# Optimization experiments

Measured on AMD Instinct MI355X. Metric: run time of the kernel, lower is better.

Reference implementation:

```python
import jax, jax.numpy as jnp
import numpy as np

N_QUBITS = 4
Q_DEPTH = 6
Q_DELTA = 0.01


def _conv1d(x, w, b):
    # x: (B, Cin, L), w: (Cout, Cin, 3), padding=1
    y = jax.lax.conv_general_dilated(x, w, window_strides=(1,), padding=[(1, 1)],
                                     dimension_numbers=('NCH', 'OIH', 'NCH'))
    return y + b[None, :, None]


def _maxpool2(x):
    B, C, L = x.shape
    return x.reshape(B, C, L // 2, 2).max(axis=-1)


def _take(state, i, axis):
    return jax.lax.index_in_dim(state, i, axis, keepdims=False)


def _apply_ry(state, theta, wire):
    # state: (B, 2, 2, 2, 2); theta: scalar (shared weight) or (B,) (per-sample)
    half = theta * 0.5
    c, s = jnp.cos(half), jnp.sin(half)
    if c.ndim == 1:  # per-sample angles -> broadcast over remaining qubit axes
        c = c.reshape(-1, 1, 1, 1)
        s = s.reshape(-1, 1, 1, 1)
    ax = wire + 1
    s0 = _take(state, 0, ax)
    s1 = _take(state, 1, ax)
    return jnp.stack([c * s0 - s * s1, s * s0 + c * s1], axis=ax)


def _apply_cnot(state, ctrl, tgt):
    cax, tax = ctrl + 1, tgt + 1
    a0 = jax.lax.slice_in_dim(state, 0, 1, axis=cax)
    a1 = jax.lax.slice_in_dim(state, 1, 2, axis=cax)
    return jnp.concatenate([a0, jnp.flip(a1, axis=tax)], axis=cax)


def _quantum_forward(q_in, q_params):
    # Batched 4-qubit state-vector simulation (PennyLane default.qubit semantics,
    # wire 0 = most significant -> axis wire+1 of (B,2,2,2,2) state).
    B = q_in.shape[0]
    # H layer on |0000> -> uniform amplitude 1/4
    state = jnp.full((B, 2, 2, 2, 2), 0.25, dtype=q_in.dtype)
    for w in range(N_QUBITS):
        state = _apply_ry(state, q_in[:, w], w)
    qw = q_params.reshape(Q_DEPTH, N_QUBITS)
    for k in range(Q_DEPTH):
        # entangling layer: CNOT(0,1), CNOT(2,3), then CNOT(1,2)
        state = _apply_cnot(state, 0, 1)
        state = _apply_cnot(state, 2, 3)
        state = _apply_cnot(state, 1, 2)
        for w in range(N_QUBITS):
            state = _apply_ry(state, qw[k, w], w)
    probs = state * state  # real amplitudes throughout (H as initial |+>^n, RY, CNOT)
    zs = [(_take(probs, 0, q + 1) - _take(probs, 1, q + 1)).sum(axis=(1, 2, 3))
          for q in range(N_QUBITS)]
    return jnp.stack(zs, axis=1)  # (B, 4) <Z_q>


def setup_inputs() -> dict:
    key = jax.random.key(0)
    ks = jax.random.split(key, 12)
    B, F = 32768, 64
    FLAT = 64 * (F // 4)  # 1024
    return {
        'x': jax.random.normal(ks[0], (B, F), jnp.float32),
        'conv1_w': jax.random.normal(ks[1], (32, 1, 3), jnp.float32) * 0.3,
        'conv1_b': jax.random.normal(ks[2], (32,), jnp.float32) * 0.05,
        'conv2_w': jax.random.normal(ks[3], (64, 32, 3), jnp.float32) * 0.05,
        'conv2_b': jax.random.normal(ks[4], (64,), jnp.float32) * 0.05,
        'fc_w': jax.random.normal(ks[5], (FLAT, 64), jnp.float32) * (1.0 / np.sqrt(FLAT)),
        'fc_b': jax.random.normal(ks[6], (64,), jnp.float32) * 0.05,
        'pre_w': jax.random.normal(ks[7], (64, N_QUBITS), jnp.float32) * 0.125,
        'pre_b': jax.random.normal(ks[8], (N_QUBITS,), jnp.float32) * 0.05,
        'q_params': Q_DELTA * jax.random.normal(ks[9], (Q_DEPTH * N_QUBITS,), jnp.float32),
        'post_w': jax.random.normal(ks[10], (N_QUBITS, 1), jnp.float32) * 0.5,
        'post_b': jax.random.normal(ks[11], (1,), jnp.float32) * 0.05,
    }


def reference(x, conv1_w, conv1_b, conv2_w, conv2_b, fc_w, fc_b,
              pre_w, pre_b, q_params, post_w, post_b):
    h = x[:, None, :]  # (B, 1, F)
    h = _maxpool2(jax.nn.relu(_conv1d(h, conv1_w, conv1_b)))   # (B, 32, F/2)
    h = _maxpool2(jax.nn.relu(_conv1d(h, conv2_w, conv2_b)))   # (B, 64, F/4)
    h = h.reshape(h.shape[0], -1)                              # (B, 1024)
    h = jax.nn.relu(h @ fc_w + fc_b)                           # (B, 64)
    q_in = jnp.tanh(h @ pre_w + pre_b) * (np.pi / 2.0)         # (B, 4)
    q_out = _quantum_forward(q_in, q_params)                   # (B, 4)
    return jax.nn.sigmoid(q_out @ post_w + post_b)             # (B, 1)
```

## Files before the change

### kernel.cpp

```cpp
#include <hip/hip_runtime.h>
#include <math.h>

typedef unsigned short u16;
typedef unsigned int u32;
typedef __attribute__((ext_vector_type(8))) short bf16x8;
typedef __attribute__((ext_vector_type(4))) float f32x4;

__device__ __forceinline__ u16 f32_to_bf16(float f) {
    u32 u = __float_as_uint(f);
    u32 r = u + 0x7FFFu + ((u >> 16) & 1u);
    return (u16)(r >> 16);
}
__device__ __forceinline__ u32 pack2(u16 a, u16 b) { return (u32)a | ((u32)b << 16); }

__device__ __forceinline__ u32 rne_bits(float f) {
    u32 u = __float_as_uint(f);
    return u + 0x7FFFu + ((u >> 16) & 1u);
}
__device__ __forceinline__ u32 pack_rne(float a, float b) {
    return __builtin_amdgcn_perm(rne_bits(b), rne_bits(a), 0x07060302u);
}

__device__ __forceinline__ float fast_tanh(float x) {
    float e = __expf(2.f * x);
    return 1.f - 2.f / (e + 1.f);
}

template<int STRIDE>
__device__ __forceinline__ void ry_gate(float st[16], float theta) {
    float s, c;
    sincosf(theta * 0.5f, &s, &c);
#pragma unroll
    for (int i = 0; i < 16; ++i) {
        if (i & STRIDE) continue;
        float s0 = st[i], s1 = st[i | STRIDE];
        st[i]          = c * s0 - s * s1;
        st[i | STRIDE] = fmaf(s, s0, c * s1);
    }
}
template<int CS, int TS>
__device__ __forceinline__ void cnot_gate(float st[16]) {
#pragma unroll
    for (int i = 0; i < 16; ++i) {
        if ((i & CS) && !(i & TS)) {
            float tmp = st[i]; st[i] = st[i | TS]; st[i | TS] = tmp;
        }
    }
}

__global__ __launch_bounds__(256) void prep_kernel(
    const float* __restrict__ fcw, const float* __restrict__ w2,
    const float* __restrict__ qp,
    u16* __restrict__ whi, u16* __restrict__ w2b, float* __restrict__ Mg)
{
    const int f  = blockIdx.x;
    const int k0 = threadIdx.x * 4;
    u16 hv[4];
#pragma unroll
    for (int i = 0; i < 4; ++i) {
        int k  = k0 + i;
        int op = k >> 6, oc = k & 63;
        hv[i] = f32_to_bf16(fcw[(size_t)(oc * 16 + op) * 64 + f]);
    }
    *(uint2*)(whi + (size_t)f * 1024 + k0) = make_uint2(pack2(hv[0], hv[1]), pack2(hv[2], hv[3]));

    if (threadIdx.x < 96) {
        const int j  = threadIdx.x;
        const int ic = j / 3, t = j - ic * 3;
        w2b[(t * 64 + f) * 32 + ic] = f32_to_bf16(w2[f * 96 + j]);
    }

    if (blockIdx.x == 0 && threadIdx.x < 16) {
        const int j = threadIdx.x;
        float st[16];
#pragma unroll
        for (int i = 0; i < 16; ++i) st[i] = (i == j) ? 1.f : 0.f;
        for (int k = 0; k < 6; ++k) {
            cnot_gate<8, 4>(st);
            cnot_gate<2, 1>(st);
            cnot_gate<4, 2>(st);
            ry_gate<8>(st, qp[k * 4 + 0]);
            ry_gate<4>(st, qp[k * 4 + 1]);
            ry_gate<2>(st, qp[k * 4 + 2]);
            ry_gate<1>(st, qp[k * 4 + 3]);
        }
#pragma unroll
        for (int i = 0; i < 16; ++i) Mg[i * 16 + j] = st[i];
    }
}

__global__ __launch_bounds__(1024, 4) void fused_kernel(
    const float* __restrict__ x,
    const float* __restrict__ w1, const float* __restrict__ b1,
    const u16* __restrict__ w2b, const float* __restrict__ b2,
    const u16* __restrict__ whi,
    const float* __restrict__ fcb,
    const float* __restrict__ prew, const float* __restrict__ preb,
    const float* __restrict__ postw, const float* __restrict__ postb,
    const float* __restrict__ Mg,
    float* __restrict__ out)
{
    __shared__ __align__(16) u16 c1h[32 * 1384];
    __shared__ float prews[256];
    __shared__ float Ms[16][17];

    const int tid  = threadIdx.x;
    const int bs   = blockIdx.x * 32;
    const int wv   = tid >> 6, lane = tid & 63;
    const int lr   = lane & 15, lq = lane >> 4;

    if (tid < 256) {
        prews[tid] = prew[tid];
        Ms[tid >> 4][tid & 15] = Mg[tid];
    }

    {
        const int s1 = tid >> 5;
        const int pp = tid & 31;
        const float* xb = x + (size_t)(bs + s1) * 64;
        const int j = 2 * pp;
        float xm1 = (j == 0)  ? 0.f : xb[j - 1];
        float x0  = xb[j];
        float x1  = xb[j + 1];
        float xp2 = (j == 62) ? 0.f : xb[j + 2];

        u16* sbase = c1h + s1 * 1384;
        if (pp == 0 || pp == 31) {
            uint4 z = make_uint4(0, 0, 0, 0);
            uint4* zr = (uint4*)(sbase + (pp == 0 ? 0 : 33) * 40);
            zr[0] = z; zr[1] = z; zr[2] = z; zr[3] = z;
        }
        u32 row[16];
#pragma unroll
        for (int icp = 0; icp < 16; ++icp) {
            float v[2];
#pragma unroll
            for (int h2 = 0; h2 < 2; ++h2) {
                int ic = icp * 2 + h2;
                float wa = w1[ic * 3], wb = w1[ic * 3 + 1], wc = w1[ic * 3 + 2], bb = b1[ic];
                float y0 = bb + wa * xm1 + wb * x0 + wc * x1;
                float y1 = bb + wa * x0  + wb * x1 + wc * xp2;
                v[h2] = fmaxf(fmaxf(y0, y1), 0.f);
            }
            row[icp] = pack_rne(v[0], v[1]);
        }
        uint4* d = (uint4*)(sbase + (1 + pp) * 40);
        d[0] = make_uint4(row[0],  row[1],  row[2],  row[3]);
        d[1] = make_uint4(row[4],  row[5],  row[6],  row[7]);
        d[2] = make_uint4(row[8],  row[9],  row[10], row[11]);
        d[3] = make_uint4(row[12], row[13], row[14], row[15]);
    }

    bf16x8 af[3][4];
#pragma unroll
    for (int t = 0; t < 3; ++t)
#pragma unroll
        for (int mt = 0; mt < 4; ++mt)
            af[t][mt] = *(const bf16x8*)(w2b + (size_t)(t * 64 + mt * 16 + lr) * 32 + lq * 8);
    f32x4 bias2[4];
#pragma unroll
    for (int mt = 0; mt < 4; ++mt)
        bias2[mt] = *(const f32x4*)(b2 + mt * 16 + lq * 4);
    __syncthreads();

#pragma unroll
    for (int nt = 0; nt < 4; ++nt) {
        const int s  = wv * 2 + (nt >> 1);
        const int qb = (nt & 1) * 16;
        const u16* bp = c1h + s * 1384 + (qb + lr) * 40 + lq * 8;
        bf16x8 bf0 = *(const bf16x8*)(bp);
        bf16x8 bf1 = *(const bf16x8*)(bp + 40);
        bf16x8 bf2 = *(const bf16x8*)(bp + 80);
        const int op = (qb + lr) >> 1;
#pragma unroll
        for (int mt = 0; mt < 4; ++mt) {
            f32x4 acc = __builtin_amdgcn_mfma_f32_16x16x32_bf16(af[0][mt], bf0, bias2[mt], 0, 0, 0);
            acc = __builtin_amdgcn_mfma_f32_16x16x32_bf16(af[1][mt], bf1, acc, 0, 0, 0);
            acc = __builtin_amdgcn_mfma_f32_16x16x32_bf16(af[2][mt], bf2, acc, 0, 0, 0);
            float p0 = fmaxf(fmaxf(acc[0], __shfl_xor(acc[0], 1)), 0.f);
            float p1 = fmaxf(fmaxf(acc[1], __shfl_xor(acc[1], 1)), 0.f);
            float p2 = fmaxf(fmaxf(acc[2], __shfl_xor(acc[2], 1)), 0.f);
            float p3 = fmaxf(fmaxf(acc[3], __shfl_xor(acc[3], 1)), 0.f);
            if (!(lane & 1)) {
                *(uint2*)(c1h + s * 1384 + op * 72 + mt * 16 + lq * 4) =
                    make_uint2(pack_rne(p0, p1), pack_rne(p2, p3));
            }
        }
    }
    __syncthreads();

    if (wv < 4) {
        const int n0 = wv * 16;
        const float fbias = fcb[n0 + lr];
        f32x4 facc0 = {0.f, 0.f, 0.f, 0.f};
        f32x4 facc1 = {0.f, 0.f, 0.f, 0.f};
        const u16* ab0 = c1h + (size_t)lr * 1384 + lq * 8;
        const u16* ab1 = c1h + (size_t)(16 + lr) * 1384 + lq * 8;
        const u16* bh  = whi + (size_t)(n0 + lr) * 1024 + lq * 8;
#pragma unroll 8
        for (int kc = 0; kc < 32; ++kc) {
            const int aoff = (kc >> 1) * 72 + (kc & 1) * 32;
            bf16x8 a0 = *(const bf16x8*)(ab0 + aoff);
            bf16x8 a1 = *(const bf16x8*)(ab1 + aoff);
            bf16x8 fh = *(const bf16x8*)(bh + kc * 32);
            facc0 = __builtin_amdgcn_mfma_f32_16x16x32_bf16(a0, fh, facc0, 0, 0, 0);
            facc1 = __builtin_amdgcn_mfma_f32_16x16x32_bf16(a1, fh, facc1, 0, 0, 0);
        }
#pragma unroll
        for (int r = 0; r < 4; ++r) {
            ((float*)(c1h + (size_t)(lq * 4 + r) * 1384 + 1152))[n0 + lr] =
                fmaxf(facc0[r] + fbias, 0.f);
            ((float*)(c1h + (size_t)(16 + lq * 4 + r) * 1384 + 1152))[n0 + lr] =
                fmaxf(facc1[r] + fbias, 0.f);
        }
    }
    __syncthreads();

    if (lane < 8) {
        const int L = lane & 3;
        const int s = wv * 2 + (lane >> 2);
        const float* hfl = (const float*)(c1h + (size_t)s * 1384 + 1152);

        float a0 = 0.f, a1 = 0.f, a2 = 0.f, a3 = 0.f;
#pragma unroll
        for (int i2 = 0; i2 < 4; ++i2) {
            float4 hv = *(const float4*)(hfl + L * 16 + i2 * 4);
#pragma unroll
            for (int c = 0; c < 4; ++c) {
                int ff = L * 16 + i2 * 4 + c;
                float4 pw = *(const float4*)&prews[ff * 4];
                float hx = (c == 0) ? hv.x : (c == 1) ? hv.y : (c == 2) ? hv.z : hv.w;
                a0 = fmaf(hx, pw.x, a0);
                a1 = fmaf(hx, pw.y, a1);
                a2 = fmaf(hx, pw.z, a2);
                a3 = fmaf(hx, pw.w, a3);
            }
        }
        a0 += __shfl_xor(a0, 1); a0 += __shfl_xor(a0, 2);
        a1 += __shfl_xor(a1, 1); a1 += __shfl_xor(a1, 2);
        a2 += __shfl_xor(a2, 1); a2 += __shfl_xor(a2, 2);
        a3 += __shfl_xor(a3, 1); a3 += __shfl_xor(a3, 2);

        const float HP = 1.5707963267948966f;
        float qin[4] = { fast_tanh(a0 + preb[0]) * HP, fast_tanh(a1 + preb[1]) * HP,
                         fast_tanh(a2 + preb[2]) * HP, fast_tanh(a3 + preb[3]) * HP };

        float va[4], vb[4];
        const float RS = 0.70710678118654752f;
#pragma unroll
        for (int w = 0; w < 4; ++w) {
            float sw, cw;
            __sincosf(qin[w] * 0.5f, &sw, &cw);
            va[w] = (cw - sw) * RS;
            vb[w] = (sw + cw) * RS;
        }
        float sv[16];
#pragma unroll
        for (int jj = 0; jj < 16; ++jj) {
            float t = (jj & 8) ? vb[0] : va[0];
            t *= (jj & 4) ? vb[1] : va[1];
            t *= (jj & 2) ? vb[2] : va[2];
            t *= (jj & 1) ? vb[3] : va[3];
            sv[jj] = t;
        }
        float z0 = 0.f, z1 = 0.f, z2 = 0.f, z3 = 0.f;
#pragma unroll
        for (int rr = 0; rr < 4; ++rr) {
            const int r = L * 4 + rr;
            float m = 0.f;
#pragma unroll
            for (int jj = 0; jj < 16; ++jj) m = fmaf(Ms[r][jj], sv[jj], m);
            float p = m * m;
            z0 += (r & 8) ? -p : p;
            z1 += (r & 4) ? -p : p;
            z2 += (r & 2) ? -p : p;
            z3 += (r & 1) ? -p : p;
        }
        z0 += __shfl_xor(z0, 1); z0 += __shfl_xor(z0, 2);
        z1 += __shfl_xor(z1, 1); z1 += __shfl_xor(z1, 2);
        z2 += __shfl_xor(z2, 1); z2 += __shfl_xor(z2, 2);
        z3 += __shfl_xor(z3, 1); z3 += __shfl_xor(z3, 2);

        if (L == 0) {
            float t = postb[0] + z0 * postw[0] + z1 * postw[1] + z2 * postw[2] + z3 * postw[3];
            out[bs + s] = 1.f / (1.f + __expf(-t));
        }
    }
}

extern "C" void kernel_launch(void* const* d_in, const int* in_sizes, int n_in,
                              void* d_out, int out_size, void* d_ws, size_t ws_size,
                              hipStream_t stream) {
    const float* x     = (const float*)d_in[0];
    const float* w1    = (const float*)d_in[1];
    const float* b1    = (const float*)d_in[2];
    const float* w2    = (const float*)d_in[3];
    const float* b2    = (const float*)d_in[4];
    const float* fcw   = (const float*)d_in[5];
    const float* fcb   = (const float*)d_in[6];
    const float* prew  = (const float*)d_in[7];
    const float* preb  = (const float*)d_in[8];
    const float* qp    = (const float*)d_in[9];
    const float* postw = (const float*)d_in[10];
    const float* postb = (const float*)d_in[11];
    float* out = (float*)d_out;

    u16*   fwhi = (u16*)d_ws;
    float* Mg   = (float*)((char*)d_ws + 131072);
    u16*   w2b  = (u16*)((char*)d_ws + 132096);

    const int B = in_sizes[0] / 64;

    prep_kernel<<<dim3(64), dim3(256), 0, stream>>>(fcw, w2, qp, fwhi, w2b, Mg);
    fused_kernel<<<dim3(B / 32), dim3(1024), 0, stream>>>(x, w1, b1, w2b, b2,
                                                          fwhi, fcb, prew, preb,
                                                          postw, postb, Mg, out);
}
```

Before: 146.4 us.

## Shrink fused kernel blocks to 8 samples and swap MFMA operand roles

The fused kernel now runs 256-thread blocks that each handle 8 samples instead of 1024-thread blocks handling 32. The shared staging buffer shrinks to match, which allows more resident blocks and more blocks in flight. The conv2 MFMA swaps its A and B operands so the maxpool pair lands inside one lane's accumulator, removing the cross-lane shuffles, though outputs are now written as scalar 16-bit stores. In the FC stage every wave runs a single MFMA with the weight as the A operand, but half of each tile's 16 columns duplicate the 8 samples, wasting MFMA work and reloading FC weights once per 8 samples instead of per 32.

```diff
diff --git a/kernel.cpp b/kernel.cpp
--- a/kernel.cpp
+++ b/kernel.cpp
@@ -16,9 +16,6 @@
 __device__ __forceinline__ u32 rne_bits(float f) {
     u32 u = __float_as_uint(f);
     return u + 0x7FFFu + ((u >> 16) & 1u);
-}
-__device__ __forceinline__ u32 pack_rne(float a, float b) {
-    return __builtin_amdgcn_perm(rne_bits(b), rne_bits(a), 0x07060302u);
 }
 
 __device__ __forceinline__ float fast_tanh(float x) {
@@ -89,7 +86,7 @@
     }
 }
 
-__global__ __launch_bounds__(1024, 4) void fused_kernel(
+__global__ __launch_bounds__(256, 5) void fused_kernel(
     const float* __restrict__ x,
     const float* __restrict__ w1, const float* __restrict__ b1,
     const u16* __restrict__ w2b, const float* __restrict__ b2,
@@ -100,19 +97,17 @@
     const float* __restrict__ Mg,
     float* __restrict__ out)
 {
-    __shared__ __align__(16) u16 c1h[32 * 1384];
+    __shared__ __align__(16) u16 c1h[8 * 1384];
     __shared__ float prews[256];
     __shared__ float Ms[16][17];
 
     const int tid  = threadIdx.x;
-    const int bs   = blockIdx.x * 32;
+    const int bs   = blockIdx.x * 8;
     const int wv   = tid >> 6, lane = tid & 63;
     const int lr   = lane & 15, lq = lane >> 4;
 
-    if (tid < 256) {
-        prews[tid] = prew[tid];
-        Ms[tid >> 4][tid & 15] = Mg[tid];
-    }
+    prews[tid] = prew[tid];
+    Ms[tid >> 4][tid & 15] = Mg[tid];
 
     {
         const int s1 = tid >> 5;
@@ -142,7 +137,7 @@
                 float y1 = bb + wa * x0  + wb * x1 + wc * xp2;
                 v[h2] = fmaxf(fmaxf(y0, y1), 0.f);
             }
-            row[icp] = pack_rne(v[0], v[1]);
+            row[icp] = __builtin_amdgcn_perm(rne_bits(v[1]), rne_bits(v[0]), 0x07060302u);
         }
         uint4* d = (uint4*)(sbase + (1 + pp) * 40);
         d[0] = make_uint4(row[0],  row[1],  row[2],  row[3]);
@@ -157,10 +152,10 @@
 #pragma unroll
         for (int mt = 0; mt < 4; ++mt)
             af[t][mt] = *(const bf16x8*)(w2b + (size_t)(t * 64 + mt * 16 + lr) * 32 + lq * 8);
-    f32x4 bias2[4];
+    float biasv[4];
 #pragma unroll
     for (int mt = 0; mt < 4; ++mt)
-        bias2[mt] = *(const f32x4*)(b2 + mt * 16 + lq * 4);
+        biasv[mt] = b2[mt * 16 + lr];
     __syncthreads();
 
 #pragma unroll
@@ -171,47 +166,40 @@
         bf16x8 bf0 = *(const bf16x8*)(bp);
         bf16x8 bf1 = *(const bf16x8*)(bp + 40);
         bf16x8 bf2 = *(const bf16x8*)(bp + 80);
-        const int op = (qb + lr) >> 1;
+        const int op0 = (qb >> 1) + lq * 2;
 #pragma unroll
         for (int mt = 0; mt < 4; ++mt) {
-            f32x4 acc = __builtin_amdgcn_mfma_f32_16x16x32_bf16(af[0][mt], bf0, bias2[mt], 0, 0, 0);
-            acc = __builtin_amdgcn_mfma_f32_16x16x32_bf16(af[1][mt], bf1, acc, 0, 0, 0);
-            acc = __builtin_amdgcn_mfma_f32_16x16x32_bf16(af[2][mt], bf2, acc, 0, 0, 0);
-            float p0 = fmaxf(fmaxf(acc[0], __shfl_xor(acc[0], 1)), 0.f);
-            float p1 = fmaxf(fmaxf(acc[1], __shfl_xor(acc[1], 1)), 0.f);
-            float p2 = fmaxf(fmaxf(acc[2], __shfl_xor(acc[2], 1)), 0.f);
-            float p3 = fmaxf(fmaxf(acc[3], __shfl_xor(acc[3], 1)), 0.f);
-            if (!(lane & 1)) {
-                *(uint2*)(c1h + s * 1384 + op * 72 + mt * 16 + lq * 4) =
-                    make_uint2(pack_rne(p0, p1), pack_rne(p2, p3));
-            }
+            f32x4 cinit = {biasv[mt], biasv[mt], biasv[mt], biasv[mt]};
+            f32x4 acc = __builtin_amdgcn_mfma_f32_16x16x32_bf16(bf0, af[0][mt], cinit, 0, 0, 0);
+            acc = __builtin_amdgcn_mfma_f32_16x16x32_bf16(bf1, af[1][mt], acc, 0, 0, 0);
+            acc = __builtin_amdgcn_mfma_f32_16x16x32_bf16(bf2, af[2][mt], acc, 0, 0, 0);
+            float p0 = fmaxf(fmaxf(acc[0], acc[1]), 0.f);
+            float p1 = fmaxf(fmaxf(acc[2], acc[3]), 0.f);
+            u16* hb = c1h + s * 1384 + mt * 16 + lr;
+            hb[(size_t)op0 * 72]       = (u16)(rne_bits(p0) >> 16);
+            hb[(size_t)(op0 + 1) * 72] = (u16)(rne_bits(p1) >> 16);
         }
     }
     __syncthreads();
 
-    if (wv < 4) {
+    {
         const int n0 = wv * 16;
-        const float fbias = fcb[n0 + lr];
-        f32x4 facc0 = {0.f, 0.f, 0.f, 0.f};
-        f32x4 facc1 = {0.f, 0.f, 0.f, 0.f};
-        const u16* ab0 = c1h + (size_t)lr * 1384 + lq * 8;
-        const u16* ab1 = c1h + (size_t)(16 + lr) * 1384 + lq * 8;
-        const u16* bh  = whi + (size_t)(n0 + lr) * 1024 + lq * 8;
+        f32x4 facc = {0.f, 0.f, 0.f, 0.f};
+        const u16* aw = whi + (size_t)(n0 + lr) * 1024 + lq * 8;
+        const u16* bh = c1h + (size_t)(lr & 7) * 1384 + lq * 8;
 #pragma unroll 8
         for (int kc = 0; kc < 32; ++kc) {
-            const int aoff = (kc >> 1) * 72 + (kc & 1) * 32;
-            bf16x8 a0 = *(const bf16x8*)(ab0 + aoff);
-            bf16x8 a1 = *(const bf16x8*)(ab1 + aoff);
-            bf16x8 fh = *(const bf16x8*)(bh + kc * 32);
-            facc0 = __builtin_amdgcn_mfma_f32_16x16x32_bf16(a0, fh, facc0, 0, 0, 0);
-            facc1 = __builtin_amdgcn_mfma_f32_16x16x32_bf16(a1, fh, facc1, 0, 0, 0);
-        }
-#pragma unroll
-        for (int r = 0; r < 4; ++r) {
-            ((float*)(c1h + (size_t)(lq * 4 + r) * 1384 + 1152))[n0 + lr] =
-                fmaxf(facc0[r] + fbias, 0.f);
-            ((float*)(c1h + (size_t)(16 + lq * 4 + r) * 1384 + 1152))[n0 + lr] =
-                fmaxf(facc1[r] + fbias, 0.f);
+            bf16x8 a = *(const bf16x8*)(aw + kc * 32);
+            bf16x8 b = *(const bf16x8*)(bh + (kc >> 1) * 72 + (kc & 1) * 32);
+            facc = __builtin_amdgcn_mfma_f32_16x16x32_bf16(a, b, facc, 0, 0, 0);
+        }
+        if (lr < 8) {
+            float4 fb = *(const float4*)(fcb + n0 + lq * 4);
+            float* hfl = (float*)(c1h + (size_t)lr * 1384 + 1152);
+            hfl[n0 + lq * 4 + 0] = fmaxf(facc[0] + fb.x, 0.f);
+            hfl[n0 + lq * 4 + 1] = fmaxf(facc[1] + fb.y, 0.f);
+            hfl[n0 + lq * 4 + 2] = fmaxf(facc[2] + fb.z, 0.f);
+            hfl[n0 + lq * 4 + 3] = fmaxf(facc[3] + fb.w, 0.f);
         }
     }
     __syncthreads();
@@ -312,7 +300,7 @@
     const int B = in_sizes[0] / 64;
 
     prep_kernel<<<dim3(64), dim3(256), 0, stream>>>(fcw, w2, qp, fwhi, w2b, Mg);
-    fused_kernel<<<dim3(B / 32), dim3(1024), 0, stream>>>(x, w1, b1, w2b, b2,
-                                                          fwhi, fcb, prew, preb,
-                                                          postw, postb, Mg, out);
-}
+    fused_kernel<<<dim3(B / 8), dim3(256), 0, stream>>>(x, w1, b1, w2b, b2,
+                                                        fwhi, fcb, prew, preb,
+                                                        postw, postb, Mg, out);
+}
```

After: 161.2 us. 1.1x slower.
